# Kernel tuning notes

Hardware: AMD Instinct MI355X
Metric: run time of the kernel (lower is better)

## Reference

```python
import jax, jax.numpy as jnp
import numpy as np

NUM_GROUPS1 = 8
NUM_GROUPS2 = 4
NUM_HEADS = 8


def setup_inputs() -> dict:
    key = jax.random.key(0)
    k1, k2, k3 = jax.random.split(key, 3)
    B, N, C = 8, 4096, 512
    x = jax.random.normal(k1, (B, N, C), dtype=jnp.float32)
    # torch Linear(dim, 3*inner_dim, bias=False); stored transposed for x @ W
    W_qkv = jax.random.normal(k2, (C, 3 * C), dtype=jnp.float32) * 0.02
    W_proj = jax.random.normal(k3, (C, C), dtype=jnp.float32) * 0.02
    b_proj = jnp.zeros((C,), dtype=jnp.float32)
    return {"x": x, "W_qkv": W_qkv, "W_proj": W_proj, "b_proj": b_proj,
            "recursive_index": 0}


def reference(x, W_qkv, W_proj, b_proj, recursive_index):
    # recursive_index is a static Python int (0 -> False branch, num_groups1).
    num_groups = NUM_GROUPS1 if not recursive_index else NUM_GROUPS2
    B, N, C = x.shape
    H = NUM_HEADS
    Dh = C // H
    scale = Dh ** -0.5
    Np = int(np.ceil(N / num_groups) * num_groups)
    if Np != N:
        x = jnp.pad(x, ((0, 0), (0, Np - N), (0, 0)))
    L = Np // num_groups  # tokens per group
    # qkv projection, then split into per-group per-head tensors [B,G,H,L,Dh]
    qkv = (x @ W_qkv).reshape(B, num_groups, L, 3, H, Dh)
    q = jnp.transpose(qkv[:, :, :, 0], (0, 1, 3, 2, 4))
    k = jnp.transpose(qkv[:, :, :, 1], (0, 1, 3, 2, 4))
    v = jnp.transpose(qkv[:, :, :, 2], (0, 1, 3, 2, 4))
    attn = jax.nn.softmax(jnp.einsum('bghld,bghmd->bghlm', q, k) * scale, axis=-1)
    out = jnp.einsum('bghlm,bghmd->bghld', attn, v)  # [B,G,H,L,Dh]
    out = jnp.transpose(out, (0, 1, 3, 2, 4)).reshape(B, Np, C)[:, :N]
    return out @ W_proj + b_proj
```

## Files before the change

### kernel.cpp

```cpp
#include <hip/hip_runtime.h>
#include <hip/hip_bf16.h>

typedef __attribute__((ext_vector_type(8))) short  bf16x8;
typedef __attribute__((ext_vector_type(4))) float  f32x4;

__device__ __forceinline__ ushort f2bf(float f) {
    unsigned u = __builtin_bit_cast(unsigned, f);
    u += 0x7fffu + ((u >> 16) & 1u);
    return (ushort)(u >> 16);
}

__device__ __forceinline__ void gload_lds16(const ushort* g, ushort* l) {
    __builtin_amdgcn_global_load_lds(
        (const __attribute__((address_space(1))) void*)(g),
        (__attribute__((address_space(3))) void*)(l), 16, 0, 0);
}

__global__ __launch_bounds__(256) void cvt_bf16_kernel(
        const float* __restrict__ in, ushort* __restrict__ out, int n4) {
    int i = blockIdx.x * 256 + threadIdx.x;
    if (i >= n4) return;
    float4 f = reinterpret_cast<const float4*>(in)[i];
    ushort4 o;
    o.x = f2bf(f.x); o.y = f2bf(f.y); o.z = f2bf(f.z); o.w = f2bf(f.w);
    reinterpret_cast<ushort4*>(out)[i] = o;
}

__global__ __launch_bounds__(256) void transpose_cvt_kernel(
        const float* __restrict__ in, ushort* __restrict__ out, int Cc, int qcols) {
    int i = blockIdx.x * 256 + threadIdx.x;
    int c = i >> 9, r = i & 511;
    float v = in[(size_t)r * Cc + c];
    if (c < qcols) v *= 0.125f;
    out[i] = f2bf(v);
}

template<bool F32OUT>
__global__ __launch_bounds__(256) void gemm_bt_kernel(
        const ushort* __restrict__ A, const ushort* __restrict__ Bt,
        void* __restrict__ Cout, const float* __restrict__ bias,
        int Ncols, int K) {
    __shared__ ushort la[128 * 32];
    __shared__ ushort lb[128 * 32];
    const int tid  = threadIdx.x;
    const int mBase = blockIdx.y << 7, nBase = blockIdx.x << 7;
    const int w = tid >> 6, lane = tid & 63, ml = lane & 15, quad = lane >> 4;
    const int wr = (w >> 1) << 6, wc = (w & 1) << 6;

    const int srow   = lane >> 2;
    const int schunk = (lane & 3) ^ (srow & 3) ^ ((srow >> 2) & 3);
    const ushort* Ap = A + (size_t)(mBase + w * 32 + srow) * K + schunk * 8;
    const ushort* Bp = Bt + (size_t)(nBase + w * 32 + srow) * K + schunk * 8;
    ushort* lA0 = la + (w * 32) * 32;
    ushort* lB0 = lb + (w * 32) * 32;

    f32x4 z4 = {0.f, 0.f, 0.f, 0.f};
    f32x4 acc[4][4];
#pragma unroll
    for (int i = 0; i < 4; ++i)
#pragma unroll
        for (int j = 0; j < 4; ++j) acc[i][j] = z4;

    const int sx = ((quad ^ (ml & 3) ^ ((ml >> 2) & 3)) << 3);
    const int nkt = K >> 5;
    for (int kt = 0; kt < nkt; ++kt) {
        gload_lds16(Ap,          lA0);
        gload_lds16(Ap + 16 * K, lA0 + 16 * 32);
        gload_lds16(Bp,          lB0);
        gload_lds16(Bp + 16 * K, lB0 + 16 * 32);
        Ap += 32; Bp += 32;
        __syncthreads();
        bf16x8 af[4], bv[4];
#pragma unroll
        for (int i = 0; i < 4; ++i)
            af[i] = *reinterpret_cast<bf16x8*>(la + (wr + i * 16 + ml) * 32 + sx);
#pragma unroll
        for (int j = 0; j < 4; ++j)
            bv[j] = *reinterpret_cast<bf16x8*>(lb + (wc + j * 16 + ml) * 32 + sx);
#pragma unroll
        for (int i = 0; i < 4; ++i)
#pragma unroll
            for (int j = 0; j < 4; ++j)
                acc[i][j] = __builtin_amdgcn_mfma_f32_16x16x32_bf16(af[i], bv[j], acc[i][j], 0, 0, 0);
        __syncthreads();
    }
#pragma unroll
    for (int i = 0; i < 4; ++i)
#pragma unroll
        for (int j = 0; j < 4; ++j)
#pragma unroll
            for (int r = 0; r < 4; ++r) {
                int row = mBase + wr + i * 16 + quad * 4 + r;
                int col = nBase + wc + j * 16 + ml;
                float v = acc[i][j][r];
                if (F32OUT)
                    reinterpret_cast<float*>(Cout)[(size_t)row * Ncols + col] = v + bias[col];
                else
                    reinterpret_cast<ushort*>(Cout)[(size_t)row * Ncols + col] = f2bf(v);
            }
}

__global__ __launch_bounds__(256) void attn_kernel(
        const ushort* __restrict__ qkv, ushort* __restrict__ out) {
    __shared__ ushort k_lds[32 * 72];
    __shared__ ushort v_lds[64 * 40];
    __shared__ ushort p_lds[4 * 32 * 40];
    const int tid = threadIdx.x;
    const int w = tid >> 6, lane = tid & 63, ml = lane & 15, quad = lane >> 4;
    const int id = blockIdx.x;
    const int bgh = id >> 2, qc = id & 3;
    const int b = bgh >> 6, g = (bgh >> 3) & 7, h = bgh & 7;
    const int tb = b * 4096 + g * 512;
    const ushort* base = qkv + (size_t)tb * 1536 + h * 64;
    const int qOff = qc * 128 + w * 32;

    bf16x8 qf[2][2];
#pragma unroll
    for (int qb = 0; qb < 2; ++qb)
#pragma unroll
        for (int ks = 0; ks < 2; ++ks)
            qf[qb][ks] = *reinterpret_cast<const bf16x8*>(
                base + (size_t)(qOff + qb * 16 + ml) * 1536 + ks * 32 + quad * 8);

    f32x4 z4 = {0.f, 0.f, 0.f, 0.f};
    f32x4 oacc[2][4];
    float lp[2][4];
#pragma unroll
    for (int qb = 0; qb < 2; ++qb) {
#pragma unroll
        for (int db = 0; db < 4; ++db) oacc[qb][db] = z4;
#pragma unroll
        for (int r = 0; r < 4; ++r) lp[qb][r] = 0.f;
    }

    ushort* pw = p_lds + w * 32 * 40;
    for (int kt = 0; kt < 16; ++kt) {
        {
            int krow = tid >> 3, dc = (tid & 7) << 3;
            *reinterpret_cast<bf16x8*>(k_lds + krow * 72 + dc) =
                *reinterpret_cast<const bf16x8*>(
                    base + (size_t)(kt * 32 + krow) * 1536 + 512 + dc);
            int dcol = tid & 63, krb = (tid >> 6) << 3;
            bf16x8 pack;
#pragma unroll
            for (int i = 0; i < 8; ++i)
                pack[i] = (short)base[(size_t)(kt * 32 + krb + i) * 1536 + 1024 + dcol];
            *reinterpret_cast<bf16x8*>(v_lds + dcol * 40 + krb) = pack;
        }
        __syncthreads();

        bf16x8 kf[2][2];
#pragma unroll
        for (int kb = 0; kb < 2; ++kb)
#pragma unroll
            for (int ks = 0; ks < 2; ++ks)
                kf[kb][ks] = *reinterpret_cast<bf16x8*>(
                    k_lds + (kb * 16 + ml) * 72 + ks * 32 + quad * 8);
        f32x4 s[2][2];
#pragma unroll
        for (int qb = 0; qb < 2; ++qb)
#pragma unroll
            for (int kb = 0; kb < 2; ++kb) {
                f32x4 t = z4;
                t = __builtin_amdgcn_mfma_f32_16x16x32_bf16(qf[qb][0], kf[kb][0], t, 0, 0, 0);
                t = __builtin_amdgcn_mfma_f32_16x16x32_bf16(qf[qb][1], kf[kb][1], t, 0, 0, 0);
                s[qb][kb] = t;
            }

#pragma unroll
        for (int qb = 0; qb < 2; ++qb)
#pragma unroll
            for (int r = 0; r < 4; ++r) {
                float p0 = __expf(s[qb][0][r]);
                float p1 = __expf(s[qb][1][r]);
                lp[qb][r] += p0 + p1;
                pw[(qb * 16 + quad * 4 + r) * 40 + ml]      = f2bf(p0);
                pw[(qb * 16 + quad * 4 + r) * 40 + 16 + ml] = f2bf(p1);
            }

        bf16x8 pf[2], vf[4];
#pragma unroll
        for (int qb = 0; qb < 2; ++qb)
            pf[qb] = *reinterpret_cast<bf16x8*>(pw + (qb * 16 + ml) * 40 + quad * 8);
#pragma unroll
        for (int db = 0; db < 4; ++db)
            vf[db] = *reinterpret_cast<bf16x8*>(v_lds + (db * 16 + ml) * 40 + quad * 8);
#pragma unroll
        for (int qb = 0; qb < 2; ++qb)
#pragma unroll
            for (int db = 0; db < 4; ++db)
                oacc[qb][db] = __builtin_amdgcn_mfma_f32_16x16x32_bf16(pf[qb], vf[db], oacc[qb][db], 0, 0, 0);
        __syncthreads();
    }

#pragma unroll
    for (int qb = 0; qb < 2; ++qb) {
        float inv[4];
#pragma unroll
        for (int r = 0; r < 4; ++r) {
            float sline = lp[qb][r];
            sline += __shfl_xor(sline, 1);
            sline += __shfl_xor(sline, 2);
            sline += __shfl_xor(sline, 4);
            sline += __shfl_xor(sline, 8);
            inv[r] = 1.0f / sline;
        }
#pragma unroll
        for (int db = 0; db < 4; ++db)
#pragma unroll
            for (int r = 0; r < 4; ++r) {
                float v = oacc[qb][db][r] * inv[r];
                out[(size_t)(tb + qOff + qb * 16 + quad * 4 + r) * 512
                    + h * 64 + db * 16 + ml] = f2bf(v);
            }
    }
}

extern "C" void kernel_launch(void* const* d_in, const int* in_sizes, int n_in,
                              void* d_out, int out_size, void* d_ws, size_t ws_size,
                              hipStream_t stream) {
    const float* x     = (const float*)d_in[0];
    const float* Wqkv  = (const float*)d_in[1];
    const float* Wproj = (const float*)d_in[2];
    const float* bproj = (const float*)d_in[3];

    char* ws = (char*)d_ws;
    ushort* xb   = (ushort*)(ws);
    ushort* wq   = (ushort*)(ws + 33554432);
    ushort* wp   = (ushort*)(ws + 35127296);
    ushort* qkv  = (ushort*)(ws + 35651584);
    ushort* attn = xb;
    float*  outp = (float*)d_out;

    cvt_bf16_kernel<<<16384, 256, 0, stream>>>(x, xb, 4194304);
    transpose_cvt_kernel<<<3072, 256, 0, stream>>>(Wqkv, wq, 1536, 512);
    transpose_cvt_kernel<<<1024, 256, 0, stream>>>(Wproj, wp, 512, 0);
    gemm_bt_kernel<false><<<dim3(12, 256), 256, 0, stream>>>(xb, wq, qkv, nullptr, 1536, 512);
    attn_kernel<<<2048, 256, 0, stream>>>(qkv, attn);
    gemm_bt_kernel<true><<<dim3(4, 256), 256, 0, stream>>>(attn, wp, outp, bproj, 512, 512);
}
```

Measured before the change: 318.6 us.

## Emit transposed V from QKV GEMM, use direct LDS loads in attention

The QKV GEMM epilogue now stages results through LDS. It writes Q/K as a packed 1024-column buffer and writes V already transposed per group and head, so attention can load K and V tiles with global_load_lds and swizzled LDS layouts instead of strided scalar gathers. The softmax folds log2(e) into the Q scale and uses exp2f. Both GEMM epilogues now issue vectorized coalesced stores, and the weight transpose uses a tiled LDS transpose. This adds epilogue LDS traffic and a second workspace buffer in exchange for removing the uncoalesced V gathers in the attention inner loop.

```diff
diff --git a/kernel.cpp b/kernel.cpp
--- a/kernel.cpp
+++ b/kernel.cpp
@@ -27,21 +27,35 @@
 }
 
 __global__ __launch_bounds__(256) void transpose_cvt_kernel(
-        const float* __restrict__ in, ushort* __restrict__ out, int Cc, int qcols) {
-    int i = blockIdx.x * 256 + threadIdx.x;
-    int c = i >> 9, r = i & 511;
-    float v = in[(size_t)r * Cc + c];
-    if (c < qcols) v *= 0.125f;
-    out[i] = f2bf(v);
-}
-
-template<bool F32OUT>
+        const float* __restrict__ in, ushort* __restrict__ out,
+        int Cc, int qcols, float qscale) {
+    __shared__ ushort t[64 * 65];
+    const int cBase = blockIdx.x * 64, rBase = blockIdx.y * 64;
+#pragma unroll
+    for (int p = 0; p < 16; ++p) {
+        int lin = p * 256 + threadIdx.x;
+        int r = lin >> 6, c = lin & 63;
+        float v = in[(size_t)(rBase + r) * Cc + cBase + c];
+        if (cBase + c < qcols) v *= qscale;
+        t[c * 65 + r] = f2bf(v);
+    }
+    __syncthreads();
+#pragma unroll
+    for (int p = 0; p < 16; ++p) {
+        int lin = p * 256 + threadIdx.x;
+        int c = lin >> 6, r = lin & 63;
+        out[(size_t)(cBase + c) * 512 + rBase + r] = t[c * 65 + r];
+    }
+}
+
+template<bool F32OUT, bool EMIT_VT>
 __global__ __launch_bounds__(256) void gemm_bt_kernel(
         const ushort* __restrict__ A, const ushort* __restrict__ Bt,
         void* __restrict__ Cout, const float* __restrict__ bias,
-        int Ncols, int K) {
-    __shared__ ushort la[128 * 32];
-    __shared__ ushort lb[128 * 32];
+        ushort* __restrict__ vT, int Ncols, int K) {
+    __shared__ ushort smem[8704];
+    ushort* la = smem;
+    ushort* lb = smem + 4096;
     const int tid  = threadIdx.x;
     const int mBase = blockIdx.y << 7, nBase = blockIdx.x << 7;
     const int w = tid >> 6, lane = tid & 63, ml = lane & 15, quad = lane >> 4;
@@ -84,26 +98,68 @@
                 acc[i][j] = __builtin_amdgcn_mfma_f32_16x16x32_bf16(af[i], bv[j], acc[i][j], 0, 0, 0);
         __syncthreads();
     }
-#pragma unroll
-    for (int i = 0; i < 4; ++i)
-#pragma unroll
-        for (int j = 0; j < 4; ++j)
-#pragma unroll
-            for (int r = 0; r < 4; ++r) {
-                int row = mBase + wr + i * 16 + quad * 4 + r;
-                int col = nBase + wc + j * 16 + ml;
-                float v = acc[i][j][r];
-                if (F32OUT)
-                    reinterpret_cast<float*>(Cout)[(size_t)row * Ncols + col] = v + bias[col];
-                else
-                    reinterpret_cast<ushort*>(Cout)[(size_t)row * Ncols + col] = f2bf(v);
-            }
+
+    if (F32OUT) {
+        float* ep = reinterpret_cast<float*>(smem) + w * 1088;
+        float bj[4];
+#pragma unroll
+        for (int j = 0; j < 4; ++j) bj[j] = bias[nBase + wc + j * 16 + ml];
+        float* cbase = reinterpret_cast<float*>(Cout);
+#pragma unroll
+        for (int i = 0; i < 4; ++i) {
+#pragma unroll
+            for (int j = 0; j < 4; ++j)
+#pragma unroll
+                for (int r = 0; r < 4; ++r)
+                    ep[(quad * 4 + r) * 68 + j * 16 + ml] = acc[i][j][r] + bj[j];
+#pragma unroll
+            for (int t = 0; t < 4; ++t) {
+                int ch = quad + 4 * t;
+                float4 v = *reinterpret_cast<const float4*>(ep + ml * 68 + ch * 4);
+                *reinterpret_cast<float4*>(cbase
+                    + (size_t)(mBase + wr + i * 16 + ml) * Ncols + nBase + wc + ch * 4) = v;
+            }
+        }
+    } else {
+        ushort* ep = smem + w * 1152;
+        const bool vblk = EMIT_VT && (nBase >= 1024);
+#pragma unroll
+        for (int i = 0; i < 4; ++i) {
+#pragma unroll
+            for (int j = 0; j < 4; ++j)
+#pragma unroll
+                for (int r = 0; r < 4; ++r)
+                    ep[(quad * 4 + r) * 72 + j * 16 + ml] = f2bf(acc[i][j][r]);
+            if (!vblk) {
+#pragma unroll
+                for (int t = 0; t < 2; ++t) {
+                    int ch = quad + 4 * t;
+                    bf16x8 v = *reinterpret_cast<const bf16x8*>(ep + ml * 72 + ch * 8);
+                    *reinterpret_cast<bf16x8*>(reinterpret_cast<ushort*>(Cout)
+                        + (size_t)(mBase + wr + i * 16 + ml) * Ncols + nBase + wc + ch * 8) = v;
+                }
+            } else {
+#pragma unroll
+                for (int t = 0; t < 2; ++t) {
+                    bf16x8 p;
+#pragma unroll
+                    for (int k = 0; k < 8; ++k)
+                        p[k] = (short)ep[(t * 8 + k) * 72 + lane];
+                    int tok = mBase + wr + i * 16 + t * 8;
+                    int vg  = (nBase - 1024) + wc + lane;
+                    *reinterpret_cast<bf16x8*>(vT
+                        + ((size_t)((tok >> 9) * 512 + vg)) * 512 + (tok & 511)) = p;
+                }
+            }
+        }
+    }
 }
 
 __global__ __launch_bounds__(256) void attn_kernel(
-        const ushort* __restrict__ qkv, ushort* __restrict__ out) {
-    __shared__ ushort k_lds[32 * 72];
-    __shared__ ushort v_lds[64 * 40];
+        const ushort* __restrict__ qk, const ushort* __restrict__ vT,
+        ushort* __restrict__ out) {
+    __shared__ ushort k_lds[32 * 64];
+    __shared__ ushort v_lds[64 * 32];
     __shared__ ushort p_lds[4 * 32 * 40];
     const int tid = threadIdx.x;
     const int w = tid >> 6, lane = tid & 63, ml = lane & 15, quad = lane >> 4;
@@ -111,7 +167,8 @@
     const int bgh = id >> 2, qc = id & 3;
     const int b = bgh >> 6, g = (bgh >> 3) & 7, h = bgh & 7;
     const int tb = b * 4096 + g * 512;
-    const ushort* base = qkv + (size_t)tb * 1536 + h * 64;
+    const ushort* base  = qk + (size_t)tb * 1024 + h * 64;
+    const ushort* vbase = vT + ((size_t)((b * 8 + g) * 512 + h * 64)) * 512;
     const int qOff = qc * 128 + w * 32;
 
     bf16x8 qf[2][2];
@@ -120,7 +177,16 @@
 #pragma unroll
         for (int ks = 0; ks < 2; ++ks)
             qf[qb][ks] = *reinterpret_cast<const bf16x8*>(
-                base + (size_t)(qOff + qb * 16 + ml) * 1536 + ks * 32 + quad * 8);
+                base + (size_t)(qOff + qb * 16 + ml) * 1024 + ks * 32 + quad * 8);
+
+    const int krl = lane >> 3;
+    const int kch = (lane & 7) ^ krl;
+    const ushort* kp = base + (size_t)(w * 8 + krl) * 1024 + 512 + kch * 8;
+    ushort* kdst = k_lds + (w * 8) * 64;
+    const int vrl = lane >> 2;
+    const int vch = (lane & 3) ^ (vrl & 3) ^ ((vrl >> 2) & 3);
+    const ushort* vp = vbase + (size_t)(w * 16 + vrl) * 512 + vch * 8;
+    ushort* vdst = v_lds + (w * 16) * 32;
 
     f32x4 z4 = {0.f, 0.f, 0.f, 0.f};
     f32x4 oacc[2][4];
@@ -133,20 +199,12 @@
         for (int r = 0; r < 4; ++r) lp[qb][r] = 0.f;
     }
 
+    const int ksw = ml & 7;
+    const int vsw = (ml & 3) ^ ((ml >> 2) & 3);
     ushort* pw = p_lds + w * 32 * 40;
     for (int kt = 0; kt < 16; ++kt) {
-        {
-            int krow = tid >> 3, dc = (tid & 7) << 3;
-            *reinterpret_cast<bf16x8*>(k_lds + krow * 72 + dc) =
-                *reinterpret_cast<const bf16x8*>(
-                    base + (size_t)(kt * 32 + krow) * 1536 + 512 + dc);
-            int dcol = tid & 63, krb = (tid >> 6) << 3;
-            bf16x8 pack;
-#pragma unroll
-            for (int i = 0; i < 8; ++i)
-                pack[i] = (short)base[(size_t)(kt * 32 + krb + i) * 1536 + 1024 + dcol];
-            *reinterpret_cast<bf16x8*>(v_lds + dcol * 40 + krb) = pack;
-        }
+        gload_lds16(kp + (size_t)kt * 32 * 1024, kdst);
+        gload_lds16(vp + kt * 32, vdst);
         __syncthreads();
 
         bf16x8 kf[2][2];
@@ -155,7 +213,7 @@
 #pragma unroll
             for (int ks = 0; ks < 2; ++ks)
                 kf[kb][ks] = *reinterpret_cast<bf16x8*>(
-                    k_lds + (kb * 16 + ml) * 72 + ks * 32 + quad * 8);
+                    k_lds + (kb * 16 + ml) * 64 + (((ks * 4 + quad) ^ ksw) << 3));
         f32x4 s[2][2];
 #pragma unroll
         for (int qb = 0; qb < 2; ++qb)
@@ -171,8 +229,8 @@
         for (int qb = 0; qb < 2; ++qb)
 #pragma unroll
             for (int r = 0; r < 4; ++r) {
-                float p0 = __expf(s[qb][0][r]);
-                float p1 = __expf(s[qb][1][r]);
+                float p0 = exp2f(s[qb][0][r]);
+                float p1 = exp2f(s[qb][1][r]);
                 lp[qb][r] += p0 + p1;
                 pw[(qb * 16 + quad * 4 + r) * 40 + ml]      = f2bf(p0);
                 pw[(qb * 16 + quad * 4 + r) * 40 + 16 + ml] = f2bf(p1);
@@ -184,7 +242,8 @@
             pf[qb] = *reinterpret_cast<bf16x8*>(pw + (qb * 16 + ml) * 40 + quad * 8);
 #pragma unroll
         for (int db = 0; db < 4; ++db)
-            vf[db] = *reinterpret_cast<bf16x8*>(v_lds + (db * 16 + ml) * 40 + quad * 8);
+            vf[db] = *reinterpret_cast<bf16x8*>(
+                v_lds + (db * 16 + ml) * 32 + ((quad ^ vsw) << 3));
 #pragma unroll
         for (int qb = 0; qb < 2; ++qb)
 #pragma unroll
@@ -228,14 +287,18 @@
     ushort* xb   = (ushort*)(ws);
     ushort* wq   = (ushort*)(ws + 33554432);
     ushort* wp   = (ushort*)(ws + 35127296);
-    ushort* qkv  = (ushort*)(ws + 35651584);
+    ushort* qkb  = (ushort*)(ws + 35651584);
+    ushort* vTb  = (ushort*)(ws + 102760448);
     ushort* attn = xb;
     float*  outp = (float*)d_out;
 
     cvt_bf16_kernel<<<16384, 256, 0, stream>>>(x, xb, 4194304);
-    transpose_cvt_kernel<<<3072, 256, 0, stream>>>(Wqkv, wq, 1536, 512);
-    transpose_cvt_kernel<<<1024, 256, 0, stream>>>(Wproj, wp, 512, 0);
-    gemm_bt_kernel<false><<<dim3(12, 256), 256, 0, stream>>>(xb, wq, qkv, nullptr, 1536, 512);
-    attn_kernel<<<2048, 256, 0, stream>>>(qkv, attn);
-    gemm_bt_kernel<true><<<dim3(4, 256), 256, 0, stream>>>(attn, wp, outp, bproj, 512, 512);
-}
+    transpose_cvt_kernel<<<dim3(24, 8), 256, 0, stream>>>(
+        Wqkv, wq, 1536, 512, 0.18033688011112043f);
+    transpose_cvt_kernel<<<dim3(8, 8), 256, 0, stream>>>(Wproj, wp, 512, 0, 1.0f);
+    gemm_bt_kernel<false, true><<<dim3(12, 256), 256, 0, stream>>>(
+        xb, wq, qkb, nullptr, vTb, 1024, 512);
+    attn_kernel<<<2048, 256, 0, stream>>>(qkb, vTb, attn);
+    gemm_bt_kernel<true, false><<<dim3(4, 256), 256, 0, stream>>>(
+        attn, wp, outp, bproj, nullptr, 512, 512);
+}
```

Result: slower. 328.0 us (+3.0%).
